# Performance work log

Hardware: AMD Instinct MI355X
Metric: run time of the kernel (lower is better)

## Reference

```python
import jax, jax.numpy as jnp
import numpy as np

B, S, D = 2, 2048, 2048
H, HD = 16, 128  # n_heads, head_dim = dim // n_heads
NEG_INF = -1e9


def setup_inputs() -> dict:
    key = jax.random.key(0)
    ks = jax.random.split(key, 6)
    x = jax.random.normal(ks[0], (B, S, D), dtype=jnp.float32)
    # freqs_complex as (real, imag) pairs; unused downstream because the
    # source's apply_rotary_emb returns its input unchanged (x.type_as(x)).
    freqs_complex = jax.random.normal(ks[1], (S, HD // 2, 2), dtype=jnp.float32)
    # causal additive mask [1, 1, S, S]
    causal = jnp.tril(jnp.ones((S, S), dtype=bool))
    mask = jnp.where(causal, 0.0, NEG_INF).astype(jnp.float32)[None, None]
    wq = jax.random.normal(ks[2], (D, D), dtype=jnp.float32) * 0.02
    wk = jax.random.normal(ks[3], (D, D), dtype=jnp.float32) * 0.02
    wv = jax.random.normal(ks[4], (D, D), dtype=jnp.float32) * 0.02
    wo = jax.random.normal(ks[5], (D, D), dtype=jnp.float32) * 0.02
    return {"x": x, "freqs_complex": freqs_complex, "mask": mask,
            "wq": wq, "wk": wk, "wv": wv, "wo": wo}


def reference(x, freqs_complex, mask, wq, wk, wv, wo):
    b, s, d = x.shape
    # QKV projections (torch Linear: x @ W.T), reshape to [B, S, H, HD]
    q = (x @ wq.T).reshape(b, s, H, HD)
    k = (x @ wk.T).reshape(b, s, H, HD)
    v = (x @ wv.T).reshape(b, s, H, HD)
    # apply_rotary_emb in the source returns its input unchanged -> no-op.
    scale = 1.0 / jnp.sqrt(jnp.asarray(HD, dtype=x.dtype))
    scores = jnp.einsum('bshd,bthd->bhst', q, k) * scale + mask
    probs = jax.nn.softmax(scores.astype(jnp.float32), axis=-1).astype(q.dtype)
    out = jnp.einsum('bhst,bthd->bshd', probs, v).reshape(b, s, H * HD)
    return out @ wo.T
```

## Files before the change

kernel.cpp:

```cpp
#include <hip/hip_runtime.h>
#include <hip/hip_bf16.h>
#include <stdint.h>


namespace {

constexpr int kB = 2;
constexpr int kS = 2048;
constexpr int kD = 2048;
constexpr int kH = 16;
constexpr int kHD = 128;
constexpr int kM = kB * kS;

typedef __attribute__((ext_vector_type(8))) __bf16 bf16x8;
typedef __attribute__((ext_vector_type(4))) float f32x4;

__device__ __forceinline__ unsigned short f2bf(float x) {
  uint32_t u = __float_as_uint(x);
  u += 0x7fffu + ((u >> 16) & 1u);
  return (unsigned short)(u >> 16);
}

__device__ __forceinline__ void gld_lds16(const void* g, void* l) {
  __builtin_amdgcn_global_load_lds((__attribute__((address_space(1))) void*)g,
                                   (__attribute__((address_space(3))) void*)l,
                                   16, 0, 0);
}

__global__ void cvt_all(const float* __restrict__ x, const float* __restrict__ wq,
                        const float* __restrict__ wk, const float* __restrict__ wv,
                        const float* __restrict__ wo, unsigned short* __restrict__ xb,
                        unsigned short* __restrict__ wqkv) {
  constexpr int n4 = kD * kD / 4;
  const int i = blockIdx.x * blockDim.x + threadIdx.x;
  const int y = blockIdx.y;
  const float* src;
  unsigned short* dst;
  float s = 1.0f;
  if (y < 2) {
    src = x + (size_t)y * n4 * 4;
    dst = xb + (size_t)y * n4 * 4;
  } else {
    src = (y == 2) ? wq : (y == 3) ? wk : (y == 4) ? wv : wo;
    dst = wqkv + (size_t)(y - 2) * n4 * 4;
    if (y == 2) s = 0.08838834764831845f * 1.44269504088896340736f;
  }
  float4 v = ((const float4*)src)[i];
  ushort4 o;
  o.x = f2bf(v.x * s); o.y = f2bf(v.y * s); o.z = f2bf(v.z * s); o.w = f2bf(v.w * s);
  ((ushort4*)dst)[i] = o;
}

template <bool OUT_BF16>
__global__ __launch_bounds__(256, 2) void gemm_bt(
    const unsigned short* __restrict__ A, const unsigned short* __restrict__ W,
    void* __restrict__ C, int M, int N, int K) {
  __shared__ unsigned short Asm[128 * 64];
  __shared__ unsigned short Bsm[128 * 64];
  const int t = threadIdx.x;
  const int wave = t >> 6, lane = t & 63;
  const int ln = lane & 15, quad = lane >> 4;
  const int wr = wave >> 1, wc = wave & 1;
  const int m0 = blockIdx.y * 128, n0 = blockIdx.x * 128;

  const int srow = t >> 3;
  const int scol = ((t & 7) ^ (srow & 7)) << 3;
  const unsigned short* gA = A + (size_t)(m0 + srow) * K + scol;
  const unsigned short* gW = W + (size_t)(n0 + srow) * K + scol;
  const size_t g32 = (size_t)32 * K;
  unsigned short* lA = Asm + wave * 512;
  unsigned short* lB = Bsm + wave * 512;

  f32x4 acc[4][4] = {};

  for (int k0 = 0; k0 < K; k0 += 64) {
    __syncthreads();
#pragma unroll
    for (int i = 0; i < 4; ++i) {
      gld_lds16(gA + i * g32, lA + i * 2048);
      gld_lds16(gW + i * g32, lB + i * 2048);
    }
    gA += 64; gW += 64;
    __syncthreads();

#pragma unroll
    for (int kk = 0; kk < 2; ++kk) {
      bf16x8 af[4], bw[4];
#pragma unroll
      for (int mt = 0; mt < 4; ++mt) {
        const int row = wr * 64 + mt * 16 + ln;
        af[mt] = *(const bf16x8*)(Asm + row * 64 +
                                  (((kk * 4 + quad) ^ (row & 7)) << 3));
      }
#pragma unroll
      for (int nt = 0; nt < 4; ++nt) {
        const int row = wc * 64 + nt * 16 + ln;
        bw[nt] = *(const bf16x8*)(Bsm + row * 64 +
                                  (((kk * 4 + quad) ^ (row & 7)) << 3));
      }
#pragma unroll
      for (int mt = 0; mt < 4; ++mt)
#pragma unroll
        for (int nt = 0; nt < 4; ++nt)
          acc[mt][nt] = __builtin_amdgcn_mfma_f32_16x16x32_bf16(
              af[mt], bw[nt], acc[mt][nt], 0, 0, 0);
    }
  }

  const int cm = m0 + wr * 64 + quad * 4;
  const int cn = n0 + wc * 64 + ln;
#pragma unroll
  for (int mt = 0; mt < 4; ++mt)
#pragma unroll
    for (int r = 0; r < 4; ++r) {
      const size_t rowoff = (size_t)(cm + mt * 16 + r) * N + cn;
      if (OUT_BF16) {
        unsigned short* Cb = (unsigned short*)C;
#pragma unroll
        for (int nt = 0; nt < 4; ++nt) Cb[rowoff + nt * 16] = f2bf(acc[mt][nt][r]);
      } else {
        float* Cf = (float*)C;
#pragma unroll
        for (int nt = 0; nt < 4; ++nt) Cf[rowoff + nt * 16] = acc[mt][nt][r];
      }
    }
}

__global__ __launch_bounds__(256, 2) void gemm_qkv(
    const unsigned short* __restrict__ A, const unsigned short* __restrict__ W,
    unsigned short* __restrict__ Qb, unsigned short* __restrict__ Kb,
    unsigned short* __restrict__ Vt) {
  constexpr int K = 2048;
  __shared__ unsigned short Asm[128 * 64];
  __shared__ unsigned short Bsm[128 * 64];
  const int t = threadIdx.x;
  const int wave = t >> 6, lane = t & 63;
  const int ln = lane & 15, quad = lane >> 4;
  const int wr = wave >> 1, wc = wave & 1;
  const int m0 = blockIdx.y * 128, n0 = blockIdx.x * 128;

  const int srow = t >> 3;
  const int scol = ((t & 7) ^ (srow & 7)) << 3;
  const unsigned short* gA = A + (size_t)(m0 + srow) * K + scol;
  const unsigned short* gW = W + (size_t)(n0 + srow) * K + scol;
  const size_t g32 = (size_t)32 * K;
  unsigned short* lA = Asm + wave * 512;
  unsigned short* lB = Bsm + wave * 512;

  f32x4 acc[4][4] = {};

  for (int k0 = 0; k0 < K; k0 += 64) {
    __syncthreads();
#pragma unroll
    for (int i = 0; i < 4; ++i) {
      gld_lds16(gA + i * g32, lA + i * 2048);
      gld_lds16(gW + i * g32, lB + i * 2048);
    }
    gA += 64; gW += 64;
    __syncthreads();

#pragma unroll
    for (int kk = 0; kk < 2; ++kk) {
      bf16x8 af[4], bw[4];
#pragma unroll
      for (int mt = 0; mt < 4; ++mt) {
        const int row = wr * 64 + mt * 16 + ln;
        af[mt] = *(const bf16x8*)(Asm + row * 64 +
                                  (((kk * 4 + quad) ^ (row & 7)) << 3));
      }
#pragma unroll
      for (int nt = 0; nt < 4; ++nt) {
        const int row = wc * 64 + nt * 16 + ln;
        bw[nt] = *(const bf16x8*)(Bsm + row * 64 +
                                  (((kk * 4 + quad) ^ (row & 7)) << 3));
      }
#pragma unroll
      for (int mt = 0; mt < 4; ++mt)
#pragma unroll
        for (int nt = 0; nt < 4; ++nt)
          acc[mt][nt] = __builtin_amdgcn_mfma_f32_16x16x32_bf16(
              af[mt], bw[nt], acc[mt][nt], 0, 0, 0);
    }
  }

  const int cm = m0 + wr * 64 + quad * 4;
  const int cn = n0 + wc * 64 + ln;
  if (n0 < 4096) {
    unsigned short* dst = (n0 < 2048) ? Qb : Kb;
    const int cnl = cn & 2047;
#pragma unroll
    for (int mt = 0; mt < 4; ++mt)
#pragma unroll
      for (int r = 0; r < 4; ++r) {
        const size_t rowoff = (size_t)(cm + mt * 16 + r) * kD + cnl;
#pragma unroll
        for (int nt = 0; nt < 4; ++nt) dst[rowoff + nt * 16] = f2bf(acc[mt][nt][r]);
      }
  } else {
#pragma unroll
    for (int mt = 0; mt < 4; ++mt)
#pragma unroll
      for (int r = 0; r < 4; ++r) {
        const int m = cm + mt * 16 + r;
        const int bb = m >> 11, s = m & 2047;
#pragma unroll
        for (int nt = 0; nt < 4; ++nt) {
          const int d = cn + nt * 16 - 4096;
          Vt[((size_t)(bb * 2048 + d)) * (size_t)kS + s] = f2bf(acc[mt][nt][r]);
        }
      }
  }
}

__global__ __launch_bounds__(256, 3) void flash_attn(
    const unsigned short* __restrict__ Q, const unsigned short* __restrict__ Kb,
    const unsigned short* __restrict__ Vt, unsigned short* __restrict__ Ob) {
  __shared__ unsigned short Ksm[64 * 128];
  __shared__ unsigned short Vsm[128 * 64];
  __shared__ unsigned short Psm[4][2048];
  const int t = threadIdx.x;
  const int wave = t >> 6, lane = t & 63;
  const int ln = lane & 15, quad = lane >> 4;
  const int bx = blockIdx.x;
  const int gq = bx >> 5;
  const int qt = (gq < 8) ? (15 - gq) : (gq - 8);
  const int bh = bx & 31, b = bh >> 4, h = bh & 15;
  const int q0 = qt * 128;

  bf16x8 qf[2][4];
#pragma unroll
  for (int st = 0; st < 2; ++st) {
    const size_t qoff =
        ((size_t)(b * kS + q0 + st * 64 + wave * 16 + ln)) * kD + h * kHD;
#pragma unroll
    for (int ks = 0; ks < 4; ++ks)
      qf[st][ks] = *(const bf16x8*)(Q + qoff + ks * 32 + quad * 8);
  }

  float lsum[2] = {0.0f, 0.0f};
  f32x4 oa[2][8] = {};

  const int krow = t >> 4;
  const unsigned short* gK =
      Kb + ((size_t)(b * kS) + krow) * kD + h * kHD + (((t & 15) ^ krow) << 3);
  const int vrow = t >> 3;
  const unsigned short* gV =
      Vt + ((size_t)(bh * 128 + vrow)) * kS + (((t & 7) ^ (vrow & 7)) << 3);

  const int nIter = 2 * qt + 2;

  for (int it = 0; it < nIter; ++it) {
    const int kv0 = it << 6;
    __syncthreads();
#pragma unroll
    for (int i = 0; i < 4; ++i)
      gld_lds16(gK + ((size_t)kv0 + i * 16) * kD, Ksm + i * 2048 + wave * 512);
#pragma unroll
    for (int i = 0; i < 4; ++i)
      gld_lds16(gV + (size_t)i * 32 * kS + kv0, Vsm + i * 2048 + wave * 512);
    __syncthreads();

    f32x4 sc[2][4] = {};
#pragma unroll
    for (int ct = 0; ct < 4; ++ct) {
      const int row = ct * 16 + ln;
#pragma unroll
      for (int ks = 0; ks < 4; ++ks) {
        bf16x8 kf =
            *(const bf16x8*)(Ksm + row * 128 + (((ks * 4 + quad) ^ ln) << 3));
#pragma unroll
        for (int st = 0; st < 2; ++st)
          sc[st][ct] = __builtin_amdgcn_mfma_f32_16x16x32_bf16(
              kf, qf[st][ks], sc[st][ct], 0, 0, 0);
      }
    }

#pragma unroll
    for (int st = 0; st < 2; ++st) {
      const int q_lo = q0 + st * 64 + wave * 16;
      const bool full = (kv0 + 63 <= q_lo);
      const int qs = q_lo + ln;
      float ls = 0.0f;
#pragma unroll
      for (int ct = 0; ct < 4; ++ct) {
        const int kvb = kv0 + ct * 16 + quad * 4;
        float p[4];
#pragma unroll
        for (int r = 0; r < 4; ++r) {
          float s = sc[st][ct][r];
          if (!full && (kvb + r > qs)) s = -1e30f;
          p[r] = exp2f(s);
          ls += p[r];
        }
        const uint32_t u0 = (uint32_t)f2bf(p[0]) | ((uint32_t)f2bf(p[1]) << 16);
        const uint32_t u1 = (uint32_t)f2bf(p[2]) | ((uint32_t)f2bf(p[3]) << 16);
        const int cs = (ct * 4 + quad) ^ (ln & 14);
        uint2 u; u.x = u0; u.y = u1;
        *(uint2*)(&Psm[wave][(st * 16 + ln) * 64 + cs * 4]) = u;
      }
      lsum[st] += ls;
    }

    bf16x8 pf[2][2];
#pragma unroll
    for (int st = 0; st < 2; ++st)
#pragma unroll
      for (int ks = 0; ks < 2; ++ks)
        pf[st][ks] = *(const bf16x8*)(
            &Psm[wave][(st * 16 + ln) * 64 +
                       (((ks * 8 + quad * 2) ^ (ln & 14)) << 2)]);
#pragma unroll
    for (int ct = 0; ct < 8; ++ct) {
      const int row = ct * 16 + ln;
#pragma unroll
      for (int ks = 0; ks < 2; ++ks) {
        bf16x8 vf =
            *(const bf16x8*)(Vsm + row * 64 + (((ks * 4 + quad) ^ (ln & 7)) << 3));
#pragma unroll
        for (int st = 0; st < 2; ++st)
          oa[st][ct] = __builtin_amdgcn_mfma_f32_16x16x32_bf16(
              pf[st][ks], vf, oa[st][ct], 0, 0, 0);
      }
    }
  }

#pragma unroll
  for (int st = 0; st < 2; ++st) {
    float l = lsum[st];
    l += __shfl_xor(l, 16, 64);
    l += __shfl_xor(l, 32, 64);
    float inv[4];
#pragma unroll
    for (int r = 0; r < 4; ++r)
      inv[r] = 1.0f / __shfl(l, (lane & 48) | (quad * 4 + r), 64);
#pragma unroll
    for (int r = 0; r < 4; ++r) {
      const size_t orow =
          ((size_t)(b * kS + q0 + st * 64 + wave * 16 + quad * 4 + r)) * kD +
          h * kHD + ln;
#pragma unroll
      for (int ct = 0; ct < 8; ++ct) Ob[orow + ct * 16] = f2bf(oa[st][ct][r] * inv[r]);
    }
  }
}

}

extern "C" void kernel_launch(void* const* d_in, const int* in_sizes, int n_in,
                              void* d_out, int out_size, void* d_ws, size_t ws_size,
                              hipStream_t stream) {
  (void)in_sizes; (void)n_in; (void)out_size; (void)ws_size;
  const float* x  = (const float*)d_in[0];
  const float* wq = (const float*)d_in[3];
  const float* wk = (const float*)d_in[4];
  const float* wv = (const float*)d_in[5];
  const float* wo = (const float*)d_in[6];
  float* out = (float*)d_out;

  unsigned short* ws   = (unsigned short*)d_ws;
  unsigned short* xb   = ws;
  unsigned short* wqkv = xb + (size_t)kM * kD;
  unsigned short* wob  = wqkv + 3 * (size_t)kD * kD;
  unsigned short* Qb   = wob + (size_t)kD * kD;
  unsigned short* Kbuf = Qb  + (size_t)kM * kD;
  unsigned short* Vt   = Kbuf + (size_t)kM * kD;
  unsigned short* Ab   = Vt + (size_t)kM * kD;

  const int n4 = kD * kD / 4;
  cvt_all<<<dim3(n4 / 256, 6), 256, 0, stream>>>(x, wq, wk, wv, wo, xb, wqkv);

  gemm_qkv<<<dim3(6144 / 128, kM / 128), 256, 0, stream>>>(xb, wqkv, Qb, Kbuf, Vt);

  flash_attn<<<dim3(512), 256, 0, stream>>>(Qb, Kbuf, Vt, Ab);

  gemm_bt<false><<<dim3(kD / 128, kM / 128), 256, 0, stream>>>(Ab, wob, out, kM, kD, kD);
}
```

Before: 372.3 us.

## Prefetch next GEMM K-tile into registers while computing current tile

Both bf16 GEMM kernels stop using direct global-to-LDS loads followed by a blocking barrier. They now load the next 64-wide K slice into registers before the MFMA work on the current slice, then write it to shared memory after a barrier. The aim is to hide global memory latency behind the matrix math. Launch bounds also rise to three blocks per CU, which may limit registers now that the extra prefetch buffers are live.

```diff
diff --git a/kernel.cpp b/kernel.cpp
--- a/kernel.cpp
+++ b/kernel.cpp
@@ -52,7 +52,7 @@
 }
 
 template <bool OUT_BF16>
-__global__ __launch_bounds__(256, 2) void gemm_bt(
+__global__ __launch_bounds__(256, 3) void gemm_bt(
     const unsigned short* __restrict__ A, const unsigned short* __restrict__ W,
     void* __restrict__ C, int M, int N, int K) {
   __shared__ unsigned short Asm[128 * 64];
@@ -68,20 +68,35 @@
   const unsigned short* gA = A + (size_t)(m0 + srow) * K + scol;
   const unsigned short* gW = W + (size_t)(n0 + srow) * K + scol;
   const size_t g32 = (size_t)32 * K;
-  unsigned short* lA = Asm + wave * 512;
-  unsigned short* lB = Bsm + wave * 512;
+  unsigned short* wAp = Asm + t * 8;
+  unsigned short* wBp = Bsm + t * 8;
 
   f32x4 acc[4][4] = {};
-
-  for (int k0 = 0; k0 < K; k0 += 64) {
-    __syncthreads();
-#pragma unroll
-    for (int i = 0; i < 4; ++i) {
-      gld_lds16(gA + i * g32, lA + i * 2048);
-      gld_lds16(gW + i * g32, lB + i * 2048);
-    }
-    gA += 64; gW += 64;
-    __syncthreads();
+  uint4 ra[4], rb[4];
+
+#pragma unroll
+  for (int i = 0; i < 4; ++i) {
+    ra[i] = *(const uint4*)(gA + i * g32);
+    rb[i] = *(const uint4*)(gW + i * g32);
+  }
+  gA += 64; gW += 64;
+#pragma unroll
+  for (int i = 0; i < 4; ++i) {
+    *(uint4*)(wAp + i * 2048) = ra[i];
+    *(uint4*)(wBp + i * 2048) = rb[i];
+  }
+
+  const int nIter = K >> 6;
+  for (int it = 0; it < nIter; ++it) {
+    __syncthreads();
+    if (it + 1 < nIter) {
+#pragma unroll
+      for (int i = 0; i < 4; ++i) {
+        ra[i] = *(const uint4*)(gA + i * g32);
+        rb[i] = *(const uint4*)(gW + i * g32);
+      }
+      gA += 64; gW += 64;
+    }
 
 #pragma unroll
     for (int kk = 0; kk < 2; ++kk) {
@@ -105,6 +120,15 @@
           acc[mt][nt] = __builtin_amdgcn_mfma_f32_16x16x32_bf16(
               af[mt], bw[nt], acc[mt][nt], 0, 0, 0);
     }
+
+    __syncthreads();
+    if (it + 1 < nIter) {
+#pragma unroll
+      for (int i = 0; i < 4; ++i) {
+        *(uint4*)(wAp + i * 2048) = ra[i];
+        *(uint4*)(wBp + i * 2048) = rb[i];
+      }
+    }
   }
 
   const int cm = m0 + wr * 64 + quad * 4;
@@ -126,7 +150,7 @@
     }
 }
 
-__global__ __launch_bounds__(256, 2) void gemm_qkv(
+__global__ __launch_bounds__(256, 3) void gemm_qkv(
     const unsigned short* __restrict__ A, const unsigned short* __restrict__ W,
     unsigned short* __restrict__ Qb, unsigned short* __restrict__ Kb,
     unsigned short* __restrict__ Vt) {
@@ -144,20 +168,35 @@
   const unsigned short* gA = A + (size_t)(m0 + srow) * K + scol;
   const unsigned short* gW = W + (size_t)(n0 + srow) * K + scol;
   const size_t g32 = (size_t)32 * K;
-  unsigned short* lA = Asm + wave * 512;
-  unsigned short* lB = Bsm + wave * 512;
+  unsigned short* wAp = Asm + t * 8;
+  unsigned short* wBp = Bsm + t * 8;
 
   f32x4 acc[4][4] = {};
-
-  for (int k0 = 0; k0 < K; k0 += 64) {
-    __syncthreads();
-#pragma unroll
-    for (int i = 0; i < 4; ++i) {
-      gld_lds16(gA + i * g32, lA + i * 2048);
-      gld_lds16(gW + i * g32, lB + i * 2048);
-    }
-    gA += 64; gW += 64;
-    __syncthreads();
+  uint4 ra[4], rb[4];
+
+#pragma unroll
+  for (int i = 0; i < 4; ++i) {
+    ra[i] = *(const uint4*)(gA + i * g32);
+    rb[i] = *(const uint4*)(gW + i * g32);
+  }
+  gA += 64; gW += 64;
+#pragma unroll
+  for (int i = 0; i < 4; ++i) {
+    *(uint4*)(wAp + i * 2048) = ra[i];
+    *(uint4*)(wBp + i * 2048) = rb[i];
+  }
+
+  const int nIter = K >> 6;
+  for (int it = 0; it < nIter; ++it) {
+    __syncthreads();
+    if (it + 1 < nIter) {
+#pragma unroll
+      for (int i = 0; i < 4; ++i) {
+        ra[i] = *(const uint4*)(gA + i * g32);
+        rb[i] = *(const uint4*)(gW + i * g32);
+      }
+      gA += 64; gW += 64;
+    }
 
 #pragma unroll
     for (int kk = 0; kk < 2; ++kk) {
@@ -180,6 +219,15 @@
         for (int nt = 0; nt < 4; ++nt)
           acc[mt][nt] = __builtin_amdgcn_mfma_f32_16x16x32_bf16(
               af[mt], bw[nt], acc[mt][nt], 0, 0, 0);
+    }
+
+    __syncthreads();
+    if (it + 1 < nIter) {
+#pragma unroll
+      for (int i = 0; i < 4; ++i) {
+        *(uint4*)(wAp + i * 2048) = ra[i];
+        *(uint4*)(wBp + i * 2048) = rb[i];
+      }
     }
   }
 
```

Measured after the change: 812.5 us. 2.18x slower.
